# Optimization experiments

Hardware: AMD Instinct MI355X
Metric: run time of the kernel (lower is better)

The kernel has to match this reference:

```python
import jax, jax.numpy as jnp
import numpy as np


def _rope_freqs(T, H, W, head_dim):
    # 3D RoPE frequency table, shape (T*H*W, head_dim)
    dim_t = head_dim - 4 * (head_dim // 6)
    dim_h = 2 * (head_dim // 6)
    dim_w = 2 * (head_dim // 6)
    base = 10000.0
    ft = 1.0 / base ** (np.arange(0, dim_t, 2)[: dim_t // 2].astype(np.float32) / dim_t)
    fh = 1.0 / base ** (np.arange(0, dim_h, 2)[: dim_h // 2].astype(np.float32) / dim_h)
    fw = 1.0 / base ** (np.arange(0, dim_w, 2)[: dim_w // 2].astype(np.float32) / dim_w)
    gt = np.arange(T, dtype=np.float32)
    gh = np.arange(H, dtype=np.float32)
    gw = np.arange(W, dtype=np.float32)
    # outer products, then repeat-interleave each freq twice: '... n -> ... (n r)', r=2
    Ft = np.repeat(gt[:, None] * ft[None, :], 2, axis=-1)  # [T, dim_t]
    Fh = np.repeat(gh[:, None] * fh[None, :], 2, axis=-1)  # [H, dim_h]
    Fw = np.repeat(gw[:, None] * fw[None, :], 2, axis=-1)  # [W, dim_w]
    Ft = np.broadcast_to(Ft[:, None, None, :], (T, H, W, Ft.shape[-1]))
    Fh = np.broadcast_to(Fh[None, :, None, :], (T, H, W, Fh.shape[-1]))
    Fw = np.broadcast_to(Fw[None, None, :, :], (T, H, W, Fw.shape[-1]))
    freqs = np.concatenate([Ft, Fh, Fw], axis=-1).reshape(T * H * W, head_dim)
    return jnp.asarray(freqs)


def _rotate_half(x):
    # pairs along last dim: (d r) with r=2 -> (-x2, x1)
    x = x.reshape(x.shape[:-1] + (x.shape[-1] // 2, 2))
    x1, x2 = x[..., 0], x[..., 1]
    return jnp.stack((-x2, x1), axis=-1).reshape(x.shape[:-2] + (-1,))


def _rms_norm(x, w, eps=1e-6):
    xf = x.astype(jnp.float32)
    y = xf * jax.lax.rsqrt(jnp.mean(xf * xf, axis=-1, keepdims=True) + eps)
    return y.astype(x.dtype) * w


def reference(x, qkv_w, qkv_b, q_norm_w, k_norm_w, proj_w, proj_b, t_size, h_size, w_size):
    B, N, C = x.shape
    Hn = 24
    D = C // Hn
    qkv = x @ qkv_w.T + qkv_b  # [B, N, 3C]
    qkv = qkv.reshape(B, N, 3, Hn, D).transpose(2, 0, 3, 1, 4)  # [3, B, H, N, D]
    q, k, v = qkv[0], qkv[1], qkv[2]
    q = _rms_norm(q, q_norm_w)
    k = _rms_norm(k, k_norm_w)
    # 3D RoPE
    freqs = _rope_freqs(int(t_size), int(h_size), int(w_size), D)  # [N, D]
    cos = jnp.cos(freqs)[None, None]  # [1,1,N,D]
    sin = jnp.sin(freqs)[None, None]
    qf, kf = q.astype(jnp.float32), k.astype(jnp.float32)
    q = (qf * cos + _rotate_half(qf) * sin).astype(q.dtype)
    k = (kf * cos + _rotate_half(kf) * sin).astype(k.dtype)
    # scaled dot-product attention
    scale = D ** -0.5
    scores = jnp.einsum('bhqd,bhkd->bhqk', q, k) * scale
    attn = jax.nn.softmax(scores, axis=-1)
    out = jnp.einsum('bhqk,bhkd->bhqd', attn, v)  # [B,H,N,D]
    out = out.transpose(0, 2, 1, 3).reshape(B, N, C)
    return out @ proj_w.T + proj_b


def setup_inputs() -> dict:
    key = jax.random.key(0)
    ks = jax.random.split(key, 6)
    B, N, C, D = 2, 2048, 3072, 128
    return {
        'x': jax.random.normal(ks[0], (B, N, C), jnp.float32),
        'qkv_w': jax.random.normal(ks[1], (3 * C, C), jnp.float32) * (C ** -0.5),
        'qkv_b': jax.random.normal(ks[2], (3 * C,), jnp.float32) * 0.02,
        'q_norm_w': jnp.ones((D,), jnp.float32),
        'k_norm_w': jnp.ones((D,), jnp.float32),
        'proj_w': jax.random.normal(ks[3], (C, C), jnp.float32) * (C ** -0.5),
        'proj_b': jax.random.normal(ks[4], (C,), jnp.float32) * 0.02,
        't_size': 8,
        'h_size': 16,
        'w_size': 16,
    }
```

## Files before the change

### kernel.cpp

```cpp
#include <hip/hip_runtime.h>
#include <math.h>

typedef __attribute__((ext_vector_type(8))) __bf16 bf16x8;
typedef __attribute__((ext_vector_type(4))) __bf16 bf16x4;
typedef __attribute__((ext_vector_type(2))) __bf16 bf16x2;
typedef __attribute__((ext_vector_type(4))) float f32x4;

#define MFMA16(a, b, c) __builtin_amdgcn_mfma_f32_16x16x32_bf16(a, b, c, 0, 0, 0)

__global__ void pack_bf16(const float* __restrict__ src, __bf16* __restrict__ dst, int n4) {
    int idx = blockIdx.x * 256 + threadIdx.x;
    if (idx < n4) {
        float4 f = *(const float4*)(src + (size_t)idx * 4);
        bf16x4 o;
        o.x = (__bf16)f.x; o.y = (__bf16)f.y; o.z = (__bf16)f.z; o.w = (__bf16)f.w;
        *(bf16x4*)(dst + (size_t)idx * 4) = o;
    }
}

template <typename OutT>
__global__ void gemm_bt_bias(const __bf16* __restrict__ A, const __bf16* __restrict__ B,
                             const float* __restrict__ bias, OutT* __restrict__ C,
                             int M, int N, int K) {
    __shared__ __align__(16) __bf16 As[128 * 72];
    __shared__ __align__(16) __bf16 Bs[128 * 72];
    const int tid = threadIdx.x;
    const int lane = tid & 63, wave = tid >> 6;
    const int lm = lane & 15, q8 = (lane >> 4) * 8, quad = lane >> 4;
    const int wr = wave >> 1, wc = wave & 1;
    const int n0 = blockIdx.x * 128, m0 = blockIdx.y * 128;

    f32x4 acc[4][4] = {};

    for (int k0 = 0; k0 < K; k0 += 64) {
        __syncthreads();
        for (int r = 0; r < 4; ++r) {
            int c = r * 256 + tid;
            int row = c >> 3, ch = (c & 7) * 8;
            uint4 ga = *(const uint4*)(A + (size_t)(m0 + row) * K + k0 + ch);
            uint4 gb = *(const uint4*)(B + (size_t)(n0 + row) * K + k0 + ch);
            *(uint4*)(As + row * 72 + ch) = ga;
            *(uint4*)(Bs + row * 72 + ch) = gb;
        }
        __syncthreads();
        for (int kk = 0; kk < 64; kk += 32) {
            bf16x8 a[4], b[4];
            for (int i = 0; i < 4; ++i)
                a[i] = *(const bf16x8*)(As + (wr * 64 + i * 16 + lm) * 72 + kk + q8);
            for (int j = 0; j < 4; ++j)
                b[j] = *(const bf16x8*)(Bs + (wc * 64 + j * 16 + lm) * 72 + kk + q8);
            for (int i = 0; i < 4; ++i)
                for (int j = 0; j < 4; ++j)
                    acc[i][j] = MFMA16(a[i], b[j], acc[i][j]);
        }
    }
    for (int j = 0; j < 4; ++j) {
        int col = n0 + wc * 64 + j * 16 + lm;
        float bj = bias[col];
        for (int i = 0; i < 4; ++i) {
            int mb = m0 + wr * 64 + i * 16 + quad * 4;
            for (int r = 0; r < 4; ++r)
                C[(size_t)(mb + r) * N + col] = (OutT)(acc[i][j][r] + bj);
        }
    }
}

__global__ void rmsrope(__bf16* __restrict__ qkv, const float* __restrict__ qw,
                        const float* __restrict__ kw) {
    int bn = blockIdx.x;
    int n = bn & 2047;
    int tid = threadIdx.x, wave = tid >> 6, lane = tid & 63;
    int d0 = lane * 2;
    int t = n >> 8, hp = (n >> 4) & 15, wp = n & 15;
    float pos, fi;
    if (d0 < 44)      { pos = (float)t;  fi = (float)(d0 >> 1) * (2.0f / 44.0f); }
    else if (d0 < 86) { pos = (float)hp; fi = (float)((d0 - 44) >> 1) * (2.0f / 42.0f); }
    else              { pos = (float)wp; fi = (float)((d0 - 86) >> 1) * (2.0f / 42.0f); }
    float freq = expf(-fi * 9.210340371976184f);
    float ang = pos * freq, sn, cs;
    sincosf(ang, &sn, &cs);
    float w0q = qw[d0], w1q = qw[d0 + 1], w0k = kw[d0], w1k = kw[d0 + 1];

    for (int h = wave; h < 24; h += 4) {
        size_t base = (size_t)bn * 9216 + h * 128 + d0;
        {
            bf16x2 xv = *(bf16x2*)(qkv + base);
            float x0 = (float)xv.x, x1 = (float)xv.y;
            float ss = x0 * x0 + x1 * x1;
            for (int m = 1; m < 64; m <<= 1) ss += __shfl_xor(ss, m, 64);
            float rr = rsqrtf(ss * (1.0f / 128.0f) + 1e-6f);
            float y0 = x0 * rr * w0q, y1 = x1 * rr * w1q;
            bf16x2 st; st.x = (__bf16)(y0 * cs - y1 * sn); st.y = (__bf16)(y1 * cs + y0 * sn);
            *(bf16x2*)(qkv + base) = st;
        }
        {
            bf16x2 xv = *(bf16x2*)(qkv + base + 3072);
            float x0 = (float)xv.x, x1 = (float)xv.y;
            float ss = x0 * x0 + x1 * x1;
            for (int m = 1; m < 64; m <<= 1) ss += __shfl_xor(ss, m, 64);
            float rr = rsqrtf(ss * (1.0f / 128.0f) + 1e-6f);
            float y0 = x0 * rr * w0k, y1 = x1 * rr * w1k;
            bf16x2 st; st.x = (__bf16)(y0 * cs - y1 * sn); st.y = (__bf16)(y1 * cs + y0 * sn);
            *(bf16x2*)(qkv + base + 3072) = st;
        }
    }
}

__global__ __launch_bounds__(256, 2)
void flash(const __bf16* __restrict__ qkv, __bf16* __restrict__ Oo) {
    __shared__ __align__(16) __bf16 Ks[64 * 136];
    __shared__ __align__(16) __bf16 VTs[128 * 72];
    __shared__ __align__(16) __bf16 Ps[128 * 72];
    int bh = blockIdx.x >> 4, qt = blockIdx.x & 15;
    int b = bh / 24, h = bh % 24;
    int q0 = qt * 128;
    int tid = threadIdx.x, wave = tid >> 6, lane = tid & 63;
    int lm = lane & 15, q8 = (lane >> 4) * 8, quad = lane >> 4;
    int wb = wave * 32;
    const float sc = 0.08838834764831845f;

    bf16x8 qf[2][4];
    for (int i = 0; i < 2; ++i)
        for (int kk = 0; kk < 4; ++kk)
            qf[i][kk] = *(const bf16x8*)(qkv + (size_t)(b * 2048 + q0 + wb + i * 16 + lm) * 9216
                                         + h * 128 + kk * 32 + q8);

    float mrow[2][4], lrow[2][4];
    f32x4 oacc[2][8] = {};
    for (int i = 0; i < 2; ++i)
        for (int r = 0; r < 4; ++r) { mrow[i][r] = -__builtin_inff(); lrow[i][r] = 0.f; }

    for (int nt = 0; nt < 32; ++nt) {
        int n0 = nt * 64;
        __syncthreads();
        for (int r = 0; r < 4; ++r) {
            int c = r * 256 + tid;
            int krow = c >> 4, kch = (c & 15) * 8;
            *(uint4*)(Ks + krow * 136 + kch) =
                *(const uint4*)(qkv + (size_t)(b * 2048 + n0 + krow) * 9216 + 3072 + h * 128 + kch);
            int vkey = c & 63, vch = (c >> 6) * 8;
            bf16x8 vv = *(const bf16x8*)(qkv + (size_t)(b * 2048 + n0 + vkey) * 9216 + 6144 + h * 128 + vch);
            for (int j = 0; j < 8; ++j)
                VTs[(vch + j) * 72 + vkey] = vv[j];
        }
        __syncthreads();

        f32x4 s[2][4] = {};
        for (int kk = 0; kk < 4; ++kk) {
            bf16x8 bk[4];
            for (int j = 0; j < 4; ++j)
                bk[j] = *(const bf16x8*)(Ks + (j * 16 + lm) * 136 + kk * 32 + q8);
            for (int i = 0; i < 2; ++i)
                for (int j = 0; j < 4; ++j)
                    s[i][j] = MFMA16(qf[i][kk], bk[j], s[i][j]);
        }
        for (int i = 0; i < 2; ++i) {
            for (int r = 0; r < 4; ++r) {
                float v0 = s[i][0][r] * sc, v1 = s[i][1][r] * sc;
                float v2 = s[i][2][r] * sc, v3 = s[i][3][r] * sc;
                float mx = fmaxf(fmaxf(v0, v1), fmaxf(v2, v3));
                for (int msk = 1; msk < 16; msk <<= 1) mx = fmaxf(mx, __shfl_xor(mx, msk, 64));
                float mn = fmaxf(mrow[i][r], mx);
                float alpha = __expf(mrow[i][r] - mn);
                float p0 = __expf(v0 - mn), p1 = __expf(v1 - mn);
                float p2 = __expf(v2 - mn), p3 = __expf(v3 - mn);
                float rs = p0 + p1 + p2 + p3;
                for (int msk = 1; msk < 16; msk <<= 1) rs += __shfl_xor(rs, msk, 64);
                lrow[i][r] = lrow[i][r] * alpha + rs;
                mrow[i][r] = mn;
                for (int ct = 0; ct < 8; ++ct) oacc[i][ct][r] *= alpha;
                int prow = wb + i * 16 + quad * 4 + r;
                Ps[prow * 72 + 0  + lm] = (__bf16)p0;
                Ps[prow * 72 + 16 + lm] = (__bf16)p1;
                Ps[prow * 72 + 32 + lm] = (__bf16)p2;
                Ps[prow * 72 + 48 + lm] = (__bf16)p3;
            }
        }
        for (int kk = 0; kk < 2; ++kk) {
            bf16x8 ap[2];
            for (int i = 0; i < 2; ++i)
                ap[i] = *(const bf16x8*)(Ps + (wb + i * 16 + lm) * 72 + kk * 32 + q8);
            for (int ct = 0; ct < 8; ++ct) {
                bf16x8 bv = *(const bf16x8*)(VTs + (ct * 16 + lm) * 72 + kk * 32 + q8);
                for (int i = 0; i < 2; ++i)
                    oacc[i][ct] = MFMA16(ap[i], bv, oacc[i][ct]);
            }
        }
    }
    for (int i = 0; i < 2; ++i) {
        for (int r = 0; r < 4; ++r) {
            float inv = 1.0f / lrow[i][r];
            int row = q0 + wb + i * 16 + quad * 4 + r;
            size_t base = ((size_t)b * 2048 + row) * 3072 + h * 128;
            for (int ct = 0; ct < 8; ++ct)
                Oo[base + ct * 16 + lm] = (__bf16)(oacc[i][ct][r] * inv);
        }
    }
}

extern "C" void kernel_launch(void* const* d_in, const int* in_sizes, int n_in,
                              void* d_out, int out_size, void* d_ws, size_t ws_size,
                              hipStream_t stream) {
    const float* x      = (const float*)d_in[0];
    const float* qkv_w  = (const float*)d_in[1];
    const float* qkv_b  = (const float*)d_in[2];
    const float* qnw    = (const float*)d_in[3];
    const float* knw    = (const float*)d_in[4];
    const float* proj_w = (const float*)d_in[5];
    const float* proj_b = (const float*)d_in[6];
    float* out = (float*)d_out;
    char* ws = (char*)d_ws;

    __bf16* xb   = (__bf16*)(ws + 0);
    __bf16* attn = (__bf16*)(ws + 0);
    __bf16* w1b  = (__bf16*)(ws + 25165824);
    __bf16* w2b  = (__bf16*)(ws + 81788928);
    __bf16* qkvb = (__bf16*)(ws + 100663296);

    pack_bf16<<<12288, 256, 0, stream>>>(x, xb, 3145728);
    pack_bf16<<<27648, 256, 0, stream>>>(qkv_w, w1b, 7077888);
    pack_bf16<<<9216, 256, 0, stream>>>(proj_w, w2b, 2359296);

    gemm_bt_bias<__bf16><<<dim3(72, 32), 256, 0, stream>>>(xb, w1b, qkv_b, qkvb, 4096, 9216, 3072);

    rmsrope<<<4096, 256, 0, stream>>>(qkvb, qnw, knw);

    flash<<<768, 256, 0, stream>>>(qkvb, attn);

    gemm_bt_bias<float><<<dim3(24, 32), 256, 0, stream>>>(attn, w2b, proj_b, out, 4096, 3072, 3072);
}
```

Baseline: 855.7 us.

## Use direct global-to-LDS loads in GEMM and transpose attention MFMA layout

The GEMM tile loads now go straight from global memory into LDS through global_load_lds, skipping the register staging step. The LDS row padding is removed so the buffer matches the contiguous layout that instruction writes, which may bring back bank conflicts on the fragment reads. In flash attention the MFMA operands are swapped so each lane holds one query row. That turns the softmax row reductions into two cross-lane shuffles, lets P and the output be written as vectors, and skips the rescale of O when no lane's running max changed.

```diff
diff --git a/kernel.cpp b/kernel.cpp
--- a/kernel.cpp
+++ b/kernel.cpp
@@ -7,6 +7,13 @@
 typedef __attribute__((ext_vector_type(4))) float f32x4;
 
 #define MFMA16(a, b, c) __builtin_amdgcn_mfma_f32_16x16x32_bf16(a, b, c, 0, 0, 0)
+
+typedef const __attribute__((address_space(1))) unsigned int* gas_t;
+typedef __attribute__((address_space(3))) unsigned int* las_t;
+
+__device__ __forceinline__ void g2lds16(const __bf16* g, __bf16* l) {
+    __builtin_amdgcn_global_load_lds((gas_t)(const void*)g, (las_t)(void*)l, 16, 0, 0);
+}
 
 __global__ void pack_bf16(const float* __restrict__ src, __bf16* __restrict__ dst, int n4) {
     int idx = blockIdx.x * 256 + threadIdx.x;
@@ -22,8 +29,8 @@
 __global__ void gemm_bt_bias(const __bf16* __restrict__ A, const __bf16* __restrict__ B,
                              const float* __restrict__ bias, OutT* __restrict__ C,
                              int M, int N, int K) {
-    __shared__ __align__(16) __bf16 As[128 * 72];
-    __shared__ __align__(16) __bf16 Bs[128 * 72];
+    __shared__ __align__(16) __bf16 As[128 * 64];
+    __shared__ __align__(16) __bf16 Bs[128 * 64];
     const int tid = threadIdx.x;
     const int lane = tid & 63, wave = tid >> 6;
     const int lm = lane & 15, q8 = (lane >> 4) * 8, quad = lane >> 4;
@@ -34,21 +41,19 @@
 
     for (int k0 = 0; k0 < K; k0 += 64) {
         __syncthreads();
-        for (int r = 0; r < 4; ++r) {
-            int c = r * 256 + tid;
+        for (int it = 0; it < 4; ++it) {
+            int c = it * 256 + tid;
             int row = c >> 3, ch = (c & 7) * 8;
-            uint4 ga = *(const uint4*)(A + (size_t)(m0 + row) * K + k0 + ch);
-            uint4 gb = *(const uint4*)(B + (size_t)(n0 + row) * K + k0 + ch);
-            *(uint4*)(As + row * 72 + ch) = ga;
-            *(uint4*)(Bs + row * 72 + ch) = gb;
+            g2lds16(A + (size_t)(m0 + row) * K + k0 + ch, As + c * 8);
+            g2lds16(B + (size_t)(n0 + row) * K + k0 + ch, Bs + c * 8);
         }
         __syncthreads();
         for (int kk = 0; kk < 64; kk += 32) {
             bf16x8 a[4], b[4];
             for (int i = 0; i < 4; ++i)
-                a[i] = *(const bf16x8*)(As + (wr * 64 + i * 16 + lm) * 72 + kk + q8);
+                a[i] = *(const bf16x8*)(As + (wr * 64 + i * 16 + lm) * 64 + kk + q8);
             for (int j = 0; j < 4; ++j)
-                b[j] = *(const bf16x8*)(Bs + (wc * 64 + j * 16 + lm) * 72 + kk + q8);
+                b[j] = *(const bf16x8*)(Bs + (wc * 64 + j * 16 + lm) * 64 + kk + q8);
             for (int i = 0; i < 4; ++i)
                 for (int j = 0; j < 4; ++j)
                     acc[i][j] = MFMA16(a[i], b[j], acc[i][j]);
@@ -125,10 +130,9 @@
             qf[i][kk] = *(const bf16x8*)(qkv + (size_t)(b * 2048 + q0 + wb + i * 16 + lm) * 9216
                                          + h * 128 + kk * 32 + q8);
 
-    float mrow[2][4], lrow[2][4];
+    float mrow[2] = {-__builtin_inff(), -__builtin_inff()};
+    float lrow[2] = {0.f, 0.f};
     f32x4 oacc[2][8] = {};
-    for (int i = 0; i < 2; ++i)
-        for (int r = 0; r < 4; ++r) { mrow[i][r] = -__builtin_inff(); lrow[i][r] = 0.f; }
 
     for (int nt = 0; nt < 32; ++nt) {
         int n0 = nt * 64;
@@ -152,29 +156,34 @@
                 bk[j] = *(const bf16x8*)(Ks + (j * 16 + lm) * 136 + kk * 32 + q8);
             for (int i = 0; i < 2; ++i)
                 for (int j = 0; j < 4; ++j)
-                    s[i][j] = MFMA16(qf[i][kk], bk[j], s[i][j]);
+                    s[i][j] = MFMA16(bk[j], qf[i][kk], s[i][j]);
         }
         for (int i = 0; i < 2; ++i) {
-            for (int r = 0; r < 4; ++r) {
-                float v0 = s[i][0][r] * sc, v1 = s[i][1][r] * sc;
-                float v2 = s[i][2][r] * sc, v3 = s[i][3][r] * sc;
-                float mx = fmaxf(fmaxf(v0, v1), fmaxf(v2, v3));
-                for (int msk = 1; msk < 16; msk <<= 1) mx = fmaxf(mx, __shfl_xor(mx, msk, 64));
-                float mn = fmaxf(mrow[i][r], mx);
-                float alpha = __expf(mrow[i][r] - mn);
-                float p0 = __expf(v0 - mn), p1 = __expf(v1 - mn);
-                float p2 = __expf(v2 - mn), p3 = __expf(v3 - mn);
-                float rs = p0 + p1 + p2 + p3;
-                for (int msk = 1; msk < 16; msk <<= 1) rs += __shfl_xor(rs, msk, 64);
-                lrow[i][r] = lrow[i][r] * alpha + rs;
-                mrow[i][r] = mn;
-                for (int ct = 0; ct < 8; ++ct) oacc[i][ct][r] *= alpha;
-                int prow = wb + i * 16 + quad * 4 + r;
-                Ps[prow * 72 + 0  + lm] = (__bf16)p0;
-                Ps[prow * 72 + 16 + lm] = (__bf16)p1;
-                Ps[prow * 72 + 32 + lm] = (__bf16)p2;
-                Ps[prow * 72 + 48 + lm] = (__bf16)p3;
+            float mx = -__builtin_inff();
+            for (int j = 0; j < 4; ++j)
+                for (int r = 0; r < 4; ++r)
+                    mx = fmaxf(mx, s[i][j][r]);
+            mx *= sc;
+            mx = fmaxf(mx, __shfl_xor(mx, 16, 64));
+            mx = fmaxf(mx, __shfl_xor(mx, 32, 64));
+            float mn = fmaxf(mrow[i], mx);
+            float alpha = __expf(mrow[i] - mn);
+            mrow[i] = mn;
+            float rs = 0.f;
+            for (int j = 0; j < 4; ++j) {
+                bf16x4 pw;
+                for (int r = 0; r < 4; ++r) {
+                    float p = __expf(s[i][j][r] * sc - mn);
+                    rs += p;
+                    pw[r] = (__bf16)p;
+                }
+                *(bf16x4*)(Ps + (wb + i * 16 + lm) * 72 + j * 16 + quad * 4) = pw;
             }
+            rs += __shfl_xor(rs, 16, 64);
+            rs += __shfl_xor(rs, 32, 64);
+            lrow[i] = lrow[i] * alpha + rs;
+            if (__any(alpha != 1.0f))
+                for (int ct = 0; ct < 8; ++ct) oacc[i][ct] *= alpha;
         }
         for (int kk = 0; kk < 2; ++kk) {
             bf16x8 ap[2];
@@ -183,17 +192,18 @@
             for (int ct = 0; ct < 8; ++ct) {
                 bf16x8 bv = *(const bf16x8*)(VTs + (ct * 16 + lm) * 72 + kk * 32 + q8);
                 for (int i = 0; i < 2; ++i)
-                    oacc[i][ct] = MFMA16(ap[i], bv, oacc[i][ct]);
+                    oacc[i][ct] = MFMA16(bv, ap[i], oacc[i][ct]);
             }
         }
     }
     for (int i = 0; i < 2; ++i) {
-        for (int r = 0; r < 4; ++r) {
-            float inv = 1.0f / lrow[i][r];
-            int row = q0 + wb + i * 16 + quad * 4 + r;
-            size_t base = ((size_t)b * 2048 + row) * 3072 + h * 128;
-            for (int ct = 0; ct < 8; ++ct)
-                Oo[base + ct * 16 + lm] = (__bf16)(oacc[i][ct][r] * inv);
+        float inv = 1.0f / lrow[i];
+        int row = q0 + wb + i * 16 + lm;
+        size_t base = ((size_t)b * 2048 + row) * 3072 + h * 128 + quad * 4;
+        for (int ct = 0; ct < 8; ++ct) {
+            bf16x4 ov;
+            for (int r = 0; r < 4; ++r) ov[r] = (__bf16)(oacc[i][ct][r] * inv);
+            *(bf16x4*)(Oo + base + ct * 16) = ov;
         }
     }
 }
```

Result: faster. 795.6 us (-7.0%).
